# Kernel tuning notes

Hardware: AMD Instinct MI355X
Metric: run time of the kernel (lower is better)

## Reference

```python
import jax, jax.numpy as jnp
import numpy as np

NUM_LAYER = 6
NUM_HEADS = 1
NEG_INF = -1e9


def setup_inputs() -> dict:
    key = jax.random.key(0)
    ks = jax.random.split(key, 8)
    bs, C, N = 8, 128, 2048
    H0 = (jax.random.uniform(ks[0], (bs, N, N)) < 0.2).astype(jnp.float32)
    vertex_feat = jax.random.normal(ks[1], (bs, C, N), dtype=jnp.float32)
    edge_feat = jax.random.normal(ks[2], (bs, C, N), dtype=jnp.float32)
    s = 1.0 / np.sqrt(C)  # Conv1d(k=1) default init scale
    Wq = jax.random.uniform(ks[3], (C, C), minval=-s, maxval=s, dtype=jnp.float32)
    bq = jax.random.uniform(ks[4], (C,), minval=-s, maxval=s, dtype=jnp.float32)
    Wk = jax.random.uniform(ks[5], (C, C), minval=-s, maxval=s, dtype=jnp.float32)
    bk = jax.random.uniform(ks[6], (C,), minval=-s, maxval=s, dtype=jnp.float32)
    return {"H0": H0, "vertex_feat": vertex_feat, "edge_feat": edge_feat,
            "Wq": Wq, "bq": bq, "Wk": Wk, "bk": bk, "it": 4}


def reference(H0, vertex_feat, edge_feat, Wq, bq, Wk, bk, it):
    bs, N, _ = H0.shape
    C = Wq.shape[0]
    head = NUM_HEADS
    dh = C // head
    # Conv1d kernel_size=1 == pointwise linear over channel dim
    Q = (jnp.einsum('oc,bcn->bon', Wq, vertex_feat) + bq[None, :, None]).reshape(bs, head, dh, N)
    K = (jnp.einsum('oc,bcn->bon', Wk, edge_feat) + bk[None, :, None]).reshape(bs, head, dh, N)
    att = jnp.einsum('bhco,bhci->bhoi', Q, K) / np.sqrt(dh)  # [bs,h,N,N]
    mask = jnp.where(H0 > 0, 0.0, NEG_INF)                   # masked_fill(1-H0)
    score = jax.nn.sigmoid(att + mask[:, None]).sum(axis=1) / head  # [bs,N,N]
    # mask_score, choice='topk': keep top-k scores per row
    k = round(N * 0.1 * (NUM_LAYER - 1 - it))
    topk_vals = jax.lax.top_k(score, k)[0]          # [bs,N,k]
    a_min = topk_vals[..., -1:]                     # k-th largest per row
    W = jnp.where(score >= a_min, score, 0.0)
    H = jnp.where(W > 0, H0, 0.0)
    # degree-normalization matrices (diag_embed of 1/deg, inf -> 0)
    deg_E = H.sum(axis=1)   # [bs,N] edge degrees
    deg_V = H.sum(axis=2)   # [bs,N] vertex degrees
    De_n_1 = jax.vmap(jnp.diag)(jnp.where(deg_E != 0, 1.0 / deg_E, 0.0))
    Dv_n_1 = jax.vmap(jnp.diag)(jnp.where(deg_V != 0, 1.0 / deg_V, 0.0))
    # edge weights: L2-normalized column sums of W (F.normalize, eps=1e-12)
    W_edge = W.sum(axis=1)
    nrm = jnp.maximum(jnp.linalg.norm(W_edge, axis=1, keepdims=True), 1e-12)
    W_edge = (W_edge / nrm)[:, :, None]  # [bs,N,1]
    return H, W, De_n_1, Dv_n_1, W_edge
```

## Files before the change

### kernel.cpp

```cpp
#include <hip/hip_runtime.h>
#include <math.h>

#define NUM_LAYER 6

typedef __attribute__((ext_vector_type(8))) short short8;
typedef __attribute__((ext_vector_type(4))) float f32x4;
typedef unsigned short u16;

__device__ __forceinline__ void split3(float x, u16& h, u16& m, u16& l) {
  unsigned ux = __float_as_uint(x);
  h = (u16)(ux >> 16);
  float r1 = x - __uint_as_float(ux & 0xFFFF0000u);
  unsigned u1 = __float_as_uint(r1);
  m = (u16)(u1 >> 16);
  float r2 = r1 - __uint_as_float(u1 & 0xFFFF0000u);
  l = (u16)(__float_as_uint(r2) >> 16);
}

__global__ __launch_bounds__(256) void qk_gemm_split(
    const float* __restrict__ Wq, const float* __restrict__ bq,
    const float* __restrict__ vf,
    const float* __restrict__ Wk, const float* __restrict__ bk,
    const float* __restrict__ ef,
    u16* __restrict__ Qh, u16* __restrict__ Qm, u16* __restrict__ Ql,
    u16* __restrict__ Kh, u16* __restrict__ Km, u16* __restrict__ Kl,
    int C, int N, int bs) {
  int which = (int)blockIdx.y >= bs;
  int b = (int)blockIdx.y - (which ? bs : 0);
  const float* Wm = which ? Wk : Wq;
  const float* bias = which ? bk : bq;
  const float* X = (which ? ef : vf) + (size_t)b * C * N;
  u16* Ph = which ? Kh : Qh;
  u16* Pm = which ? Km : Qm;
  u16* Pl = which ? Kl : Ql;
  int n0 = blockIdx.x * 128;
  __shared__ float As[8][128];
  __shared__ float Xs[8][128];
  int t = threadIdx.x;
  int tx = t & 15, ty = t >> 4;
  int ao = t >> 1, ac = (t & 1) * 4;
  int lk = t >> 5, lj = (t & 31) * 4;
  float acc[8][8] = {};
  for (int c0 = 0; c0 < C; c0 += 8) {
    __syncthreads();
    float4 wv = *(const float4*)&Wm[(size_t)ao * C + c0 + ac];
    As[ac + 0][ao] = wv.x; As[ac + 1][ao] = wv.y;
    As[ac + 2][ao] = wv.z; As[ac + 3][ao] = wv.w;
    *(float4*)&Xs[lk][lj] = *(const float4*)&X[(size_t)(c0 + lk) * N + n0 + lj];
    __syncthreads();
#pragma unroll
    for (int kk = 0; kk < 8; ++kk) {
      float a[8], bb[8];
      *(float4*)&a[0]  = *(const float4*)&As[kk][ty * 4];
      *(float4*)&a[4]  = *(const float4*)&As[kk][64 + ty * 4];
      *(float4*)&bb[0] = *(const float4*)&Xs[kk][tx * 4];
      *(float4*)&bb[4] = *(const float4*)&Xs[kk][64 + tx * 4];
#pragma unroll
      for (int i = 0; i < 8; ++i)
#pragma unroll
        for (int j = 0; j < 8; ++j)
          acc[i][j] = fmaf(a[i], bb[j], acc[i][j]);
    }
  }
  float bv[8];
#pragma unroll
  for (int i = 0; i < 8; ++i) bv[i] = bias[(i >> 2) * 64 + ty * 4 + (i & 3)];
#pragma unroll
  for (int j = 0; j < 8; ++j) {
    int n = n0 + tx * 4 + (j & 3) + (j >> 2) * 64;
    size_t nb = ((size_t)b * N + n) * C;
#pragma unroll
    for (int g = 0; g < 2; ++g) {
      int r0 = g * 64 + ty * 4;
      ushort4 hv, mv, lv;
      split3(acc[g * 4 + 0][j] + bv[g * 4 + 0], hv.x, mv.x, lv.x);
      split3(acc[g * 4 + 1][j] + bv[g * 4 + 1], hv.y, mv.y, lv.y);
      split3(acc[g * 4 + 2][j] + bv[g * 4 + 2], hv.z, mv.z, lv.z);
      split3(acc[g * 4 + 3][j] + bv[g * 4 + 3], hv.w, mv.w, lv.w);
      *(ushort4*)&Ph[nb + r0] = hv;
      *(ushort4*)&Pm[nb + r0] = mv;
      *(ushort4*)&Pl[nb + r0] = lv;
    }
  }
}

__global__ __launch_bounds__(256) void att_mfma(
    const u16* __restrict__ Qh, const u16* __restrict__ Qm,
    const u16* __restrict__ Ql, const u16* __restrict__ Kh,
    const u16* __restrict__ Km, const u16* __restrict__ Kl,
    const float* __restrict__ H0, float* __restrict__ score,
    int C, int N, float rsdh) {
  int b = blockIdx.z;
  int o0 = blockIdx.y * 128, i0 = blockIdx.x * 128;
  __shared__ u16 sm[6][128][40];
  __shared__ float et[4][16][68];
  int t = threadIdx.x;
  int wave = t >> 6, lane = t & 63, quad = lane >> 4, lr = lane & 15;
  int wo = wave >> 1, wi = wave & 1;
  f32x4 acc[4][4];
#pragma unroll
  for (int mi = 0; mi < 4; ++mi)
#pragma unroll
    for (int ni = 0; ni < 4; ++ni) acc[mi][ni] = (f32x4){0.f, 0.f, 0.f, 0.f};

  int ro = t >> 1, ch = (t & 1) * 16;
  size_t qbase = ((size_t)b * N + o0 + ro) * C + ch;
  size_t kbase = ((size_t)b * N + i0 + ro) * C + ch;
  const u16* gq[3] = {Qh, Qm, Ql};
  const u16* gk[3] = {Kh, Km, Kl};

  for (int c0 = 0; c0 < C; c0 += 32) {
    __syncthreads();
#pragma unroll
    for (int a = 0; a < 3; ++a) {
      const uint4* src = (const uint4*)(gq[a] + qbase + c0);
      *(uint4*)&sm[a][ro][ch] = src[0];
      *(uint4*)&sm[a][ro][ch + 8] = src[1];
      const uint4* srk = (const uint4*)(gk[a] + kbase + c0);
      *(uint4*)&sm[3 + a][ro][ch] = srk[0];
      *(uint4*)&sm[3 + a][ro][ch + 8] = srk[1];
    }
    __syncthreads();
    short8 bh[4], bm[4], bl[4];
#pragma unroll
    for (int ni = 0; ni < 4; ++ni) {
      int row = wi * 64 + ni * 16 + lr;
      bh[ni] = *(const short8*)&sm[3][row][quad * 8];
      bm[ni] = *(const short8*)&sm[4][row][quad * 8];
      bl[ni] = *(const short8*)&sm[5][row][quad * 8];
    }
#pragma unroll
    for (int mi = 0; mi < 4; ++mi) {
      int row = wo * 64 + mi * 16 + lr;
      short8 ah = *(const short8*)&sm[0][row][quad * 8];
      short8 am = *(const short8*)&sm[1][row][quad * 8];
      short8 al = *(const short8*)&sm[2][row][quad * 8];
#pragma unroll
      for (int ni = 0; ni < 4; ++ni) {
        f32x4 c = acc[mi][ni];
        c = __builtin_amdgcn_mfma_f32_16x16x32_bf16(ah, bl[ni], c, 0, 0, 0);
        c = __builtin_amdgcn_mfma_f32_16x16x32_bf16(al, bh[ni], c, 0, 0, 0);
        c = __builtin_amdgcn_mfma_f32_16x16x32_bf16(am, bm[ni], c, 0, 0, 0);
        c = __builtin_amdgcn_mfma_f32_16x16x32_bf16(ah, bm[ni], c, 0, 0, 0);
        c = __builtin_amdgcn_mfma_f32_16x16x32_bf16(am, bh[ni], c, 0, 0, 0);
        c = __builtin_amdgcn_mfma_f32_16x16x32_bf16(ah, bh[ni], c, 0, 0, 0);
        acc[mi][ni] = c;
      }
    }
  }
  const float* Hb = H0 + (size_t)b * N * N;
  float* Sb = score + (size_t)b * N * N;
  int rr = lane >> 2, seg = lane & 3;
#pragma unroll
  for (int mi = 0; mi < 4; ++mi) {
#pragma unroll
    for (int ni = 0; ni < 4; ++ni)
#pragma unroll
      for (int r = 0; r < 4; ++r)
        et[wave][quad * 4 + r][ni * 16 + lr] = acc[mi][ni][r];
    __syncthreads();
    int o = o0 + wo * 64 + mi * 16 + rr;
    const float* hr = Hb + (size_t)o * N + i0 + wi * 64;
    float* sr = Sb + (size_t)o * N + i0 + wi * 64;
#pragma unroll
    for (int j = 0; j < 4; ++j) {
      int col = j * 16 + seg * 4;
      float4 c = *(const float4*)&et[wave][rr][col];
      float4 h = *(const float4*)&hr[col];
      float4 oV;
      oV.x = (h.x > 0.f) ? 1.f / (1.f + __expf(-c.x * rsdh)) : 0.f;
      oV.y = (h.y > 0.f) ? 1.f / (1.f + __expf(-c.y * rsdh)) : 0.f;
      oV.z = (h.z > 0.f) ? 1.f / (1.f + __expf(-c.z * rsdh)) : 0.f;
      oV.w = (h.w > 0.f) ? 1.f / (1.f + __expf(-c.w * rsdh)) : 0.f;
      *(float4*)&sr[col] = oV;
    }
    __syncthreads();
  }
}

template <int V4>
__global__ __launch_bounds__(512) void topk_select(
    float* __restrict__ scoreW, float* __restrict__ Hout,
    float* __restrict__ degV, float* __restrict__ Dv, int dodv,
    float* __restrict__ PE, float* __restrict__ PW,
    const int* __restrict__ itp, int N) {
  int b = blockIdx.y;
  int strip = blockIdx.x;
  int t = threadIdx.x;
  int wave = t >> 6, lane = t & 63;
  int row = strip * 8 + wave;
  size_t rowoff = ((size_t)b * N + row) * N;
  extern __shared__ float cols[];
  float* colE = cols;
  float* colW = cols + N;
  for (int i = t; i < 2 * N; i += 512) cols[i] = 0.f;

  float4 v4[V4];
#pragma unroll
  for (int q = 0; q < V4; ++q)
    v4[q] = *(const float4*)(scoreW + rowoff + 4 * lane + (q << 8));
  int itv = *itp;
  int k = (int)floor((double)N * 0.1 * (double)(NUM_LAYER - 1 - itv) + 0.5);
  unsigned lo = 0u, hi = 0x3F800000u;
  while (lo < hi) {
    unsigned r = hi - lo;
    unsigned p1 = lo + (r + 2u) / 3u;
    unsigned p2 = lo + (2u * r + 2u) / 3u;
    float t1 = __uint_as_float(p1), t2 = __uint_as_float(p2);
    int c = 0;
#pragma unroll
    for (int q = 0; q < V4; ++q) {
      c += (v4[q].x >= t1) ? 1 : 0; c += (v4[q].x >= t2) ? 0x10000 : 0;
      c += (v4[q].y >= t1) ? 1 : 0; c += (v4[q].y >= t2) ? 0x10000 : 0;
      c += (v4[q].z >= t1) ? 1 : 0; c += (v4[q].z >= t2) ? 0x10000 : 0;
      c += (v4[q].w >= t1) ? 1 : 0; c += (v4[q].w >= t2) ? 0x10000 : 0;
    }
#pragma unroll
    for (int off = 1; off < 64; off <<= 1) c += __shfl_xor(c, off);
    int c2 = c >> 16, c1 = c & 0xFFFF;
    if (c2 >= k) lo = p2;
    else if (c1 >= k) { lo = p1; hi = p2 - 1u; }
    else hi = p1 - 1u;
  }
  float am = __uint_as_float(lo);
  __syncthreads();

  float rs = 0.f;
#pragma unroll
  for (int q = 0; q < V4; ++q) {
    int c0 = 4 * lane + (q << 8);
    float4 s = v4[q];
    float4 w, h;
    w.x = (s.x >= am) ? s.x : 0.f; h.x = (w.x > 0.f) ? 1.f : 0.f;
    w.y = (s.y >= am) ? s.y : 0.f; h.y = (w.y > 0.f) ? 1.f : 0.f;
    w.z = (s.z >= am) ? s.z : 0.f; h.z = (w.z > 0.f) ? 1.f : 0.f;
    w.w = (s.w >= am) ? s.w : 0.f; h.w = (w.w > 0.f) ? 1.f : 0.f;
    *(float4*)(scoreW + rowoff + c0) = w;
    *(float4*)(Hout + rowoff + c0) = h;
    rs += h.x + h.y + h.z + h.w;
    if (h.x != 0.f) { atomicAdd(&colE[c0 + 0], 1.f); atomicAdd(&colW[c0 + 0], w.x); }
    if (h.y != 0.f) { atomicAdd(&colE[c0 + 1], 1.f); atomicAdd(&colW[c0 + 1], w.y); }
    if (h.z != 0.f) { atomicAdd(&colE[c0 + 2], 1.f); atomicAdd(&colW[c0 + 2], w.z); }
    if (h.w != 0.f) { atomicAdd(&colE[c0 + 3], 1.f); atomicAdd(&colW[c0 + 3], w.w); }
  }
#pragma unroll
  for (int off = 32; off; off >>= 1) rs += __shfl_down(rs, off);
  float rsb = __shfl(rs, 0);
  if (lane == 0) degV[b * N + row] = rsb;
  if (dodv) {
    float inv = (rsb != 0.f) ? 1.f / rsb : 0.f;
    float* dvr = Dv + ((size_t)b * N + row) * N;
    for (int c4 = lane * 4; c4 < N; c4 += 256) {
      float4 z = {0.f, 0.f, 0.f, 0.f};
      unsigned dd = (unsigned)(row - c4);
      if (dd < 4u) ((float*)&z)[dd] = inv;
      *(float4*)&dvr[c4] = z;
    }
  }
  __syncthreads();
  int S = N >> 3;
  size_t pbase = ((size_t)b * S + strip) * N;
  for (int c = 4 * t; c < N; c += 2048) {
    *(float4*)(PE + pbase + c) = *(const float4*)&colE[c];
    *(float4*)(PW + pbase + c) = *(const float4*)&colW[c];
  }
}

__global__ __launch_bounds__(256) void col_reduce(
    const float* __restrict__ PE, const float* __restrict__ PW,
    float* __restrict__ degE, float* __restrict__ We, int N, int S) {
  int b = blockIdx.y;
  int l = threadIdx.x & 63;
  int sg = threadIdx.x >> 6;
  int col = blockIdx.x * 64 + l;
  int cnt = S >> 2;
  int s0 = sg * cnt;
  float se = 0.f, sw = 0.f;
  for (int i = 0; i < cnt; ++i) {
    size_t o = ((size_t)b * S + s0 + i) * N + col;
    se += PE[o];
    sw += PW[o];
  }
  __shared__ float rE[4][64], rW[4][64];
  rE[sg][l] = se;
  rW[sg][l] = sw;
  __syncthreads();
  if (sg == 0) {
    float te = rE[0][l] + rE[1][l] + rE[2][l] + rE[3][l];
    float tw = rW[0][l] + rW[1][l] + rW[2][l] + rW[3][l];
    degE[b * N + col] = te;
    We[b * N + col] = tw;
  }
}

__global__ __launch_bounds__(256) void dedv_fill(
    float* __restrict__ De, float* __restrict__ Dv,
    const float* __restrict__ degE, const float* __restrict__ degV, int N) {
  int arr = blockIdx.z;
  int b = blockIdx.y;
  int r0 = blockIdx.x * 8;
  float* out = (arr ? Dv : De) + (size_t)b * N * N;
  const float* deg = (arr ? degV : degE) + b * N;
  int t = threadIdx.x;
#pragma unroll
  for (int r = r0; r < r0 + 8; ++r) {
    float d = deg[r];
    float inv = (d != 0.f) ? 1.f / d : 0.f;
    size_t rowoff = (size_t)r * N;
    for (int c4 = t * 4; c4 < N; c4 += 1024) {
      float4 v = {0.f, 0.f, 0.f, 0.f};
      unsigned dd = (unsigned)(r - c4);
      if (dd < 4u) ((float*)&v)[dd] = inv;
      *(float4*)&out[rowoff + c4] = v;
    }
  }
}

__global__ __launch_bounds__(256) void wedge_norm(
    const float* __restrict__ We, float* __restrict__ out, int N) {
  int b = blockIdx.x;
  int t = threadIdx.x;
  const float* w = We + (size_t)b * N;
  float ss = 0.f;
  for (int i = t; i < N; i += 256) { float x = w[i]; ss += x * x; }
  for (int off = 32; off; off >>= 1) ss += __shfl_down(ss, off);
  __shared__ float p[4];
  if ((t & 63) == 0) p[t >> 6] = ss;
  __syncthreads();
  float tot = p[0] + p[1] + p[2] + p[3];
  float nrm = fmaxf(sqrtf(tot), 1e-12f);
  for (int i = t; i < N; i += 256) out[(size_t)b * N + i] = w[i] / nrm;
}

extern "C" void kernel_launch(void* const* d_in, const int* in_sizes, int n_in,
                              void* d_out, int out_size, void* d_ws, size_t ws_size,
                              hipStream_t stream) {
  const float* H0 = (const float*)d_in[0];
  const float* vf = (const float*)d_in[1];
  const float* ef = (const float*)d_in[2];
  const float* Wq = (const float*)d_in[3];
  const float* bq = (const float*)d_in[4];
  const float* Wk = (const float*)d_in[5];
  const float* bk = (const float*)d_in[6];
  const int* itp  = (const int*)d_in[7];

  int C = (int)(sqrt((double)in_sizes[3]) + 0.5);
  long long ratio = (long long)in_sizes[0] / in_sizes[1];
  int N = (int)(C * ratio);
  int bs = (int)(in_sizes[1] / ((long long)C * N));
  size_t bNN = (size_t)bs * N * N;
  size_t bNC = (size_t)bs * N * C;
  int S = N >> 3;
  size_t pElems = (size_t)bs * S * N;

  float* outH  = (float*)d_out;
  float* outW  = outH + bNN;
  float* outDe = outW + bNN;
  float* outDv = outDe + bNN;
  float* outWe = outDv + bNN;

  size_t bsN = (size_t)bs * N;
  float* degE = (float*)d_ws;
  float* degV = degE + bsN;
  float* We   = degV + bsN;
  u16* splits;
  float* PE;
  float* PW;
  int dodv;
  size_t need = 3 * bsN * sizeof(float) + 6 * bNC * sizeof(u16) +
                2 * pElems * sizeof(float);
  if (ws_size >= need) {
    splits = (u16*)(We + bsN);
    PE = (float*)(splits + 6 * bNC);
    PW = PE + pElems;
    dodv = 1;
  } else {
    splits = (u16*)outDe;
    PE = outDv;
    PW = PE + pElems;
    dodv = 0;
  }
  u16* Qh = splits;
  u16* Qm = Qh + bNC;
  u16* Ql = Qm + bNC;
  u16* Kh = Ql + bNC;
  u16* Km = Kh + bNC;
  u16* Kl = Km + bNC;

  float rsdh = (float)(1.0 / sqrt((double)C));
  size_t colsBytes = 2 * (size_t)N * sizeof(float);

  qk_gemm_split<<<dim3(N / 128, 2 * bs), 256, 0, stream>>>(
      Wq, bq, vf, Wk, bk, ef, Qh, Qm, Ql, Kh, Km, Kl, C, N, bs);
  att_mfma<<<dim3(N / 128, N / 128, bs), 256, 0, stream>>>(
      Qh, Qm, Ql, Kh, Km, Kl, H0, outW, C, N, rsdh);
  if (N == 2048)
    topk_select<8><<<dim3(S, bs), 512, colsBytes, stream>>>(
        outW, outH, degV, outDv, dodv, PE, PW, itp, N);
  else if (N == 1024)
    topk_select<4><<<dim3(S, bs), 512, colsBytes, stream>>>(
        outW, outH, degV, outDv, dodv, PE, PW, itp, N);
  else
    topk_select<16><<<dim3(S, bs), 512, colsBytes, stream>>>(
        outW, outH, degV, outDv, dodv, PE, PW, itp, N);
  col_reduce<<<dim3(N / 64, bs), 256, 0, stream>>>(PE, PW, degE, We, N, S);
  dedv_fill<<<dim3(N / 8, bs, dodv ? 1 : 2), 256, 0, stream>>>(
      outDe, outDv, degE, degV, N);
  wedge_norm<<<dim3(bs), 256, 0, stream>>>(We, outWe, N);
}
```

Measured before the change: 861.7 us.

## Write attention epilogue directly from MFMA regs and fuse De fill into col_reduce

The attention epilogue now drops its LDS transpose and the two barriers per tile. Each lane writes scalar sigmoid-masked scores straight from the MFMA accumulators, and the kernel gets a 3-blocks-per-CU launch bound plus a smaller LDS padding. The De diagonal fill moves into col_reduce, which removes a separate launch and a pass over degE. The trade-offs are less coalesced scalar H0 loads and score stores, possible LDS bank conflicts from the new padding, and fewer, longer-running blocks writing De.

```diff
diff --git a/kernel.cpp b/kernel.cpp
--- a/kernel.cpp
+++ b/kernel.cpp
@@ -84,7 +84,7 @@
   }
 }
 
-__global__ __launch_bounds__(256) void att_mfma(
+__global__ __launch_bounds__(256, 3) void att_mfma(
     const u16* __restrict__ Qh, const u16* __restrict__ Qm,
     const u16* __restrict__ Ql, const u16* __restrict__ Kh,
     const u16* __restrict__ Km, const u16* __restrict__ Kl,
@@ -92,8 +92,7 @@
     int C, int N, float rsdh) {
   int b = blockIdx.z;
   int o0 = blockIdx.y * 128, i0 = blockIdx.x * 128;
-  __shared__ u16 sm[6][128][40];
-  __shared__ float et[4][16][68];
+  __shared__ u16 sm[6][128][34];
   int t = threadIdx.x;
   int wave = t >> 6, lane = t & 63, quad = lane >> 4, lr = lane & 15;
   int wo = wave >> 1, wi = wave & 1;
@@ -150,31 +149,21 @@
   }
   const float* Hb = H0 + (size_t)b * N * N;
   float* Sb = score + (size_t)b * N * N;
-  int rr = lane >> 2, seg = lane & 3;
+  int colb = i0 + wi * 64 + lr;
 #pragma unroll
   for (int mi = 0; mi < 4; ++mi) {
 #pragma unroll
-    for (int ni = 0; ni < 4; ++ni)
-#pragma unroll
-      for (int r = 0; r < 4; ++r)
-        et[wave][quad * 4 + r][ni * 16 + lr] = acc[mi][ni][r];
-    __syncthreads();
-    int o = o0 + wo * 64 + mi * 16 + rr;
-    const float* hr = Hb + (size_t)o * N + i0 + wi * 64;
-    float* sr = Sb + (size_t)o * N + i0 + wi * 64;
-#pragma unroll
-    for (int j = 0; j < 4; ++j) {
-      int col = j * 16 + seg * 4;
-      float4 c = *(const float4*)&et[wave][rr][col];
-      float4 h = *(const float4*)&hr[col];
-      float4 oV;
-      oV.x = (h.x > 0.f) ? 1.f / (1.f + __expf(-c.x * rsdh)) : 0.f;
-      oV.y = (h.y > 0.f) ? 1.f / (1.f + __expf(-c.y * rsdh)) : 0.f;
-      oV.z = (h.z > 0.f) ? 1.f / (1.f + __expf(-c.z * rsdh)) : 0.f;
-      oV.w = (h.w > 0.f) ? 1.f / (1.f + __expf(-c.w * rsdh)) : 0.f;
-      *(float4*)&sr[col] = oV;
-    }
-    __syncthreads();
+    for (int r = 0; r < 4; ++r) {
+      int o = o0 + wo * 64 + mi * 16 + quad * 4 + r;
+      const float* hr = Hb + (size_t)o * N + colb;
+      float* sr = Sb + (size_t)o * N + colb;
+#pragma unroll
+      for (int ni = 0; ni < 4; ++ni) {
+        float h = hr[ni * 16];
+        float c = acc[mi][ni][r];
+        sr[ni * 16] = (h > 0.f) ? 1.f / (1.f + __expf(-c * rsdh)) : 0.f;
+      }
+    }
   }
 }
 
@@ -268,7 +257,8 @@
 
 __global__ __launch_bounds__(256) void col_reduce(
     const float* __restrict__ PE, const float* __restrict__ PW,
-    float* __restrict__ degE, float* __restrict__ We, int N, int S) {
+    float* __restrict__ degE, float* __restrict__ We,
+    float* __restrict__ De, int N, int S) {
   int b = blockIdx.y;
   int l = threadIdx.x & 63;
   int sg = threadIdx.x >> 6;
@@ -281,7 +271,7 @@
     se += PE[o];
     sw += PW[o];
   }
-  __shared__ float rE[4][64], rW[4][64];
+  __shared__ float rE[4][64], rW[4][64], invE[64];
   rE[sg][l] = se;
   rW[sg][l] = sw;
   __syncthreads();
@@ -290,17 +280,30 @@
     float tw = rW[0][l] + rW[1][l] + rW[2][l] + rW[3][l];
     degE[b * N + col] = te;
     We[b * N + col] = tw;
-  }
-}
-
-__global__ __launch_bounds__(256) void dedv_fill(
-    float* __restrict__ De, float* __restrict__ Dv,
-    const float* __restrict__ degE, const float* __restrict__ degV, int N) {
-  int arr = blockIdx.z;
+    invE[l] = (te != 0.f) ? 1.f / te : 0.f;
+  }
+  __syncthreads();
+  float* Deb = De + (size_t)b * N * N;
+  int t = threadIdx.x;
+  for (int rr = 0; rr < 64; ++rr) {
+    int r = blockIdx.x * 64 + rr;
+    float inv = invE[rr];
+    size_t rowo = (size_t)r * N;
+    for (int c4 = t * 4; c4 < N; c4 += 1024) {
+      float4 v = {0.f, 0.f, 0.f, 0.f};
+      unsigned dd = (unsigned)(r - c4);
+      if (dd < 4u) ((float*)&v)[dd] = inv;
+      *(float4*)&Deb[rowo + c4] = v;
+    }
+  }
+}
+
+__global__ __launch_bounds__(256) void dv_fill(
+    float* __restrict__ Dv, const float* __restrict__ degV, int N) {
   int b = blockIdx.y;
   int r0 = blockIdx.x * 8;
-  float* out = (arr ? Dv : De) + (size_t)b * N * N;
-  const float* deg = (arr ? degV : degE) + b * N;
+  float* out = Dv + (size_t)b * N * N;
+  const float* deg = degV + b * N;
   int t = threadIdx.x;
 #pragma unroll
   for (int r = r0; r < r0 + 8; ++r) {
@@ -403,8 +406,9 @@
   else
     topk_select<16><<<dim3(S, bs), 512, colsBytes, stream>>>(
         outW, outH, degV, outDv, dodv, PE, PW, itp, N);
-  col_reduce<<<dim3(N / 64, bs), 256, 0, stream>>>(PE, PW, degE, We, N, S);
-  dedv_fill<<<dim3(N / 8, bs, dodv ? 1 : 2), 256, 0, stream>>>(
-      outDe, outDv, degE, degV, N);
+  col_reduce<<<dim3(N / 64, bs), 256, 0, stream>>>(PE, PW, degE, We, outDe,
+                                                   N, S);
+  if (!dodv)
+    dv_fill<<<dim3(N / 8, bs), 256, 0, stream>>>(outDv, degV, N);
   wedge_norm<<<dim3(bs), 256, 0, stream>>>(We, outWe, N);
 }
```

Result: slower. 940.7 us (+9.2%).
